# Kernel tuning notes

Measured on AMD Instinct MI355X. Metric: run time of the kernel, lower is better.

Reference implementation:

```python
import jax, jax.numpy as jnp
import numpy as np

N = 50000      # nodes
E = 800000     # directed edges (before self-loops)
DX, DF = 128, 128   # x / feat dims, nfeat = DX + DF = 256
NHID = 256
NRES = 100     # policy head outputs NRES + 1


def setup_inputs() -> dict:
    key = jax.random.key(0)
    ks = jax.random.split(key, 12)
    def lin(k, fin, fout):
        s = 1.0 / np.sqrt(fin)
        kw, kb = jax.random.split(k)
        return (jax.random.uniform(kw, (fin, fout), jnp.float32, -s, s),
                jax.random.uniform(kb, (fout,), jnp.float32, -s, s))
    W1, b1 = lin(ks[3], DX + DF, NHID)
    W2, b2 = lin(ks[4], NHID, NHID)
    Wp, bp = lin(ks[5], NHID, NRES + 1)
    Wq, bq = lin(ks[6], NHID, 1)
    return {
        "x": jax.random.normal(ks[0], (N, DX), jnp.float32),
        "feat": jax.random.normal(ks[1], (N, DF), jnp.float32),
        "edge_index": jax.random.randint(ks[2], (2, E), 0, N, dtype=jnp.int64),
        "W1": W1, "b1": b1, "W2": W2, "b2": b2,
        "Wp": Wp, "bp": bp, "Wq": Wq, "bq": bq,
    }


def _gcn_conv(h, row, col, W, b):
    # h: [N, Fin]; row/col already include self-loops
    h = h @ W + b                                        # linear first (as in source)
    deg = jax.ops.segment_sum(jnp.ones_like(row, h.dtype), row, num_segments=N)
    dis = deg ** -0.5                                    # deg >= 1 thanks to self-loops
    norm = dis[row] * dis[col]                           # [E+N]
    # gather-scale-scatter: out[col] += norm * h[row]
    return jax.ops.segment_sum(norm[:, None] * h[row], col, num_segments=N)


def reference(x, feat, edge_index, W1, b1, W2, b2, Wp, bp, Wq, bq):
    loops = jnp.arange(N, dtype=edge_index.dtype)
    row = jnp.concatenate([edge_index[0], loops])
    col = jnp.concatenate([edge_index[1], loops])

    h = jnp.concatenate([x, feat], axis=-1)              # [N, nfeat]
    h = jax.nn.relu(_gcn_conv(h, row, col, W1, b1))      # dropout p=0 -> identity
    h = jax.nn.relu(_gcn_conv(h, row, col, W2, b2))
    g = jnp.max(h, axis=0)                               # global max pool over nodes -> [NHID]
    finx = g @ Wp + bp                                   # [NRES+1]
    finy = g @ Wq + bq                                   # [1]
    return finx, jax.nn.softmax(finx, axis=0), finy
```

## Files before the change

### kernel.cpp

```cpp
#include <hip/hip_runtime.h>

#define N_NODES 50000
#define N_EDGES 800000
#define NHID    256
#define NRES_P1 101

#define NBUCK   196
#define EPB     3125
#define BCAP    6144
#define POOL_BLOCKS 2048
#define LDK     40

typedef unsigned short u16;
typedef unsigned char  u8;
typedef unsigned long long ull;
typedef __attribute__((ext_vector_type(8))) short short8;
typedef __attribute__((ext_vector_type(4))) float f32x4;

static __device__ __forceinline__ unsigned f2bf(float f) {
    unsigned u = __float_as_uint(f);
    return (u + 0x7FFF + ((u >> 16) & 1)) >> 16;
}
static __device__ __forceinline__ float bflo(unsigned p) {
    return __uint_as_float(p << 16);
}
static __device__ __forceinline__ u8 f2fp8(float f) {
    return (u8)(__builtin_amdgcn_cvt_pk_fp8_f32(f, f, 0, false) & 0xff);
}


__global__ __launch_bounds__(256) void k_bcount(
    const int* __restrict__ ei, int* __restrict__ pC, int* __restrict__ pR) {
    __shared__ int cC[NBUCK], cR[NBUCK];
    int b = blockIdx.x, t = threadIdx.x;
    if (t < NBUCK) { cC[t] = 0; cR[t] = 0; }
    __syncthreads();
    int base = b * EPB;
    for (int i = t; i < EPB; i += 256) {
        int r = ei[base + i];
        int c = ei[N_EDGES + base + i];
        atomicAdd(&cR[r >> 8], 1);
        atomicAdd(&cC[c >> 8], 1);
    }
    __syncthreads();
    if (t < NBUCK) { pC[b * NBUCK + t] = cC[t]; pR[b * NBUCK + t] = cR[t]; }
}

__global__ __launch_bounds__(256) void k_bscan(
    const int* __restrict__ pC, const int* __restrict__ pR,
    int* __restrict__ offC, int* __restrict__ offR,
    int* __restrict__ estC, int* __restrict__ estR) {
    __shared__ int totC[NBUCK], totR[NBUCK];
    int t = threadIdx.x;
    if (t < NBUCK) {
        int runC = 0, runR = 0;
        for (int b = 0; b < 256; b += 8) {
            int vc[8], vr[8];
#pragma unroll
            for (int j = 0; j < 8; ++j) {
                vc[j] = pC[(b + j) * NBUCK + t];
                vr[j] = pR[(b + j) * NBUCK + t];
            }
#pragma unroll
            for (int j = 0; j < 8; ++j) {
                offC[t * 256 + b + j] = runC; runC += vc[j];
                offR[t * 256 + b + j] = runR; runR += vr[j];
            }
        }
        totC[t] = runC; totR[t] = runR;
    }
    __syncthreads();
    if (t == 0) {
        int rc = 0, rr = 0;
        for (int k = 0; k < NBUCK; ++k) {
            estC[k] = rc; rc += totC[k];
            estR[k] = rr; rr += totR[k];
        }
        estC[NBUCK] = rc; estR[NBUCK] = rr;
    }
}

__global__ __launch_bounds__(256) void k_bscatter(
    const int* __restrict__ ei, const int* __restrict__ offC,
    const int* __restrict__ offR, const int* __restrict__ estC,
    const int* __restrict__ estR, unsigned* __restrict__ sortC,
    u16* __restrict__ sortR) {
    __shared__ int curC[NBUCK], curR[NBUCK];
    int b = blockIdx.x, t = threadIdx.x;
    if (t < NBUCK) {
        curC[t] = estC[t] + offC[t * 256 + b];
        curR[t] = estR[t] + offR[t * 256 + b];
    }
    __syncthreads();
    int base = b * EPB;
    for (int i = t; i < EPB; i += 256) {
        int r = ei[base + i];
        int c = ei[N_EDGES + base + i];
        int pc = atomicAdd(&curC[c >> 8], 1);
        sortC[pc] = ((unsigned)(c & 255) << 16) | (unsigned)r;
        int pr = atomicAdd(&curR[r >> 8], 1);
        sortR[pr] = (u16)(r & 255);
    }
}

__global__ __launch_bounds__(256) void k_bcsr(
    const unsigned* __restrict__ sortC, const int* __restrict__ estC,
    const u16* __restrict__ sortR, const int* __restrict__ estR,
    int* __restrict__ rowptr, int* __restrict__ rowend,
    int* __restrict__ srcl, float* __restrict__ dis) {
    __shared__ int hist[256], cur[256], excl[256], hist2[256];
    __shared__ int wsum[4], woff[4];
    __shared__ unsigned stg[BCAP];
    int k = blockIdx.x, t = threadIdx.x;
    int lane = t & 63, wid = t >> 6;
    int nloc = min(256, N_NODES - k * 256);
    int es = estC[k], ee = estC[k + 1];
    int ecnt = ee - es;
    int fs = es + k * 256;
    hist[t] = 0; cur[t] = 0; hist2[t] = 0;
    __syncthreads();
    for (int i = t; i < ecnt; i += 256)
        atomicAdd(&hist[sortC[es + i] >> 16], 1);
    {
        int rs = estR[k], rcnt = estR[k + 1] - rs;
        for (int i = t; i < rcnt; i += 256)
            atomicAdd(&hist2[(int)sortR[rs + i]], 1);
    }
    __syncthreads();
    if (t < nloc) dis[k * 256 + t] = rsqrtf((float)(hist2[t] + 1));
    int sv = hist[t] + (t < nloc ? 1 : 0);
    int sc = sv;
#pragma unroll
    for (int off = 1; off < 64; off <<= 1) {
        int y = __shfl_up(sc, off, 64);
        if (lane >= off) sc += y;
    }
    if (lane == 63) wsum[wid] = sc;
    __syncthreads();
    if (t == 0) {
        int r = 0;
#pragma unroll
        for (int w = 0; w < 4; ++w) { woff[w] = r; r += wsum[w]; }
    }
    __syncthreads();
    int ex = woff[wid] + sc - sv;
    excl[t] = ex;
    if (t < nloc) {
        rowptr[k * 256 + t] = fs + ex;
        rowend[k * 256 + t] = fs + ex + hist[t] + 1;
    }
    __syncthreads();
    int tot = ecnt + nloc;
    if (tot <= BCAP) {
        for (int i = t; i < ecnt; i += 256) {
            unsigned v = sortC[es + i];
            int j = v >> 16;
            int p = excl[j] + atomicAdd(&cur[j], 1);
            stg[p] = v & 0xffffu;
        }
        if (t < nloc) stg[excl[t] + hist[t]] = (unsigned)(k * 256 + t);
        __syncthreads();
        for (int i = t; i < tot; i += 256) srcl[fs + i] = (int)stg[i];
    } else {
        for (int i = t; i < ecnt; i += 256) {
            unsigned v = sortC[es + i];
            int j = v >> 16;
            int p = excl[j] + atomicAdd(&cur[j], 1);
            srcl[fs + p] = (int)(v & 0xffffu);
        }
        if (t < nloc) srcl[fs + excl[t] + hist[t]] = k * 256 + t;
    }
}

__global__ void k_prep_w2(const float* __restrict__ W1, const float* __restrict__ W2,
                          u16* __restrict__ W1T, u16* __restrict__ W2T) {
    int tid = blockIdx.x * 256 + threadIdx.x;
    const float* W = (tid < 8192) ? W1 : W2;
    u16* WT = (tid < 8192) ? W1T : W2T;
    int id = tid & 8191;
    int n = id >> 5, k8 = (id & 31) << 3;
    u16 tmp[8];
#pragma unroll
    for (int i = 0; i < 8; ++i) tmp[i] = (u16)f2bf(W[(size_t)(k8 + i) * 256 + n]);
    *(uint4*)&WT[(size_t)n * 256 + k8] = *(uint4*)tmp;
}


template <bool SPLIT, bool W16, bool W8>
__global__ __launch_bounds__(256, 2) void k_gemm_mfma(
    const void* __restrict__ A0v, const float* __restrict__ A1,
    const u16* __restrict__ WT, const float* __restrict__ bias,
    const float* __restrict__ dis, u16* __restrict__ out16,
    u8* __restrict__ out8, int M) {
    __shared__ u16 As[128][LDK];
    __shared__ u16 Bs[256][LDK];
    const int t = threadIdx.x;
    const int m0 = blockIdx.x * 128;
    const int lane = t & 63, wave = t >> 6;
    const int wm = wave & 1, wn = wave >> 1;
    const int lr = lane & 15, kg = lane >> 4;

    f32x4 acc[4][8] = {};

    for (int k0 = 0; k0 < 256; k0 += 32) {
#pragma unroll
        for (int i = 0; i < 2; ++i) {
            int idx = i * 256 + t;
            int row = idx >> 2, kc = (idx & 3) << 3;
            int grow = m0 + row;
            uint4 pk = {0u, 0u, 0u, 0u};
            if (grow < M) {
                if (SPLIT) {
                    int k = k0 + kc;
                    const float* src = (k < 128)
                        ? ((const float*)A0v + (size_t)grow * 128 + k)
                        : (A1 + (size_t)grow * 128 + (k - 128));
                    float4 f0 = *(const float4*)src;
                    float4 f1 = *(const float4*)(src + 4);
                    pk.x = f2bf(f0.x) | (f2bf(f0.y) << 16);
                    pk.y = f2bf(f0.z) | (f2bf(f0.w) << 16);
                    pk.z = f2bf(f1.x) | (f2bf(f1.y) << 16);
                    pk.w = f2bf(f1.z) | (f2bf(f1.w) << 16);
                } else {
                    pk = *(const uint4*)((const u16*)A0v +
                                         (size_t)grow * 256 + k0 + kc);
                }
            }
            *(uint4*)&As[row][kc] = pk;
        }
#pragma unroll
        for (int i = 0; i < 4; ++i) {
            int idx = i * 256 + t;
            int n = idx >> 2, kc = (idx & 3) << 3;
            *(uint4*)&Bs[n][kc] = *(const uint4*)&WT[(size_t)n * 256 + k0 + kc];
        }
        __syncthreads();
        short8 af[4], bf[8];
#pragma unroll
        for (int mi = 0; mi < 4; ++mi)
            af[mi] = *(const short8*)&As[wm * 64 + mi * 16 + lr][kg * 8];
#pragma unroll
        for (int ni = 0; ni < 8; ++ni)
            bf[ni] = *(const short8*)&Bs[wn * 128 + ni * 16 + lr][kg * 8];
#pragma unroll
        for (int mi = 0; mi < 4; ++mi)
#pragma unroll
            for (int ni = 0; ni < 8; ++ni)
                acc[mi][ni] = __builtin_amdgcn_mfma_f32_16x16x32_bf16(
                    af[mi], bf[ni], acc[mi][ni], 0, 0, 0);
        __syncthreads();
    }

    const int orow = m0 + wm * 64;
    const int ocol = wn * 128;
#pragma unroll
    for (int mi = 0; mi < 4; ++mi) {
#pragma unroll
        for (int r = 0; r < 4; ++r) {
            int row = orow + mi * 16 + kg * 4 + r;
            if (row >= M) continue;
            float d = dis[row];
#pragma unroll
            for (int ni = 0; ni < 8; ++ni) {
                int col = ocol + ni * 16 + lr;
                float v = d * (acc[mi][ni][r] + bias[col]);
                if (W16) out16[(size_t)row * 256 + col] = (u16)f2bf(v);
                if (W8)  out8[(size_t)row * 256 + col] = f2fp8(v);
            }
        }
    }
}


static __device__ __forceinline__ void addf8(uint2 v, float* a) {
    auto f0 = __builtin_amdgcn_cvt_pk_f32_fp8((int)v.x, false);
    auto f1 = __builtin_amdgcn_cvt_pk_f32_fp8((int)v.x, true);
    auto f2 = __builtin_amdgcn_cvt_pk_f32_fp8((int)v.y, false);
    auto f3 = __builtin_amdgcn_cvt_pk_f32_fp8((int)v.y, true);
    a[0] += f0[0]; a[1] += f0[1]; a[2] += f1[0]; a[3] += f1[1];
    a[4] += f2[0]; a[5] += f2[1]; a[6] += f3[0]; a[7] += f3[1];
}

static __device__ __forceinline__ void gather_batch16_f8(
    const int* __restrict__ p, const u8* __restrict__ base, float* a) {
    int4 q0 = *(const int4*)p;
    int4 q1 = *(const int4*)(p + 4);
    int4 q2 = *(const int4*)(p + 8);
    int4 q3 = *(const int4*)(p + 12);
    uint2 v0  = *(const uint2*)(base + (size_t)q0.x * 256);
    uint2 v1  = *(const uint2*)(base + (size_t)q0.y * 256);
    uint2 v2  = *(const uint2*)(base + (size_t)q0.z * 256);
    uint2 v3  = *(const uint2*)(base + (size_t)q0.w * 256);
    uint2 v4  = *(const uint2*)(base + (size_t)q1.x * 256);
    uint2 v5  = *(const uint2*)(base + (size_t)q1.y * 256);
    uint2 v6  = *(const uint2*)(base + (size_t)q1.z * 256);
    uint2 v7  = *(const uint2*)(base + (size_t)q1.w * 256);
    uint2 v8  = *(const uint2*)(base + (size_t)q2.x * 256);
    uint2 v9  = *(const uint2*)(base + (size_t)q2.y * 256);
    uint2 v10 = *(const uint2*)(base + (size_t)q2.z * 256);
    uint2 v11 = *(const uint2*)(base + (size_t)q2.w * 256);
    uint2 v12 = *(const uint2*)(base + (size_t)q3.x * 256);
    uint2 v13 = *(const uint2*)(base + (size_t)q3.y * 256);
    uint2 v14 = *(const uint2*)(base + (size_t)q3.z * 256);
    uint2 v15 = *(const uint2*)(base + (size_t)q3.w * 256);
    addf8(v0, a);  addf8(v1, a);  addf8(v2, a);  addf8(v3, a);
    addf8(v4, a);  addf8(v5, a);  addf8(v6, a);  addf8(v7, a);
    addf8(v8, a);  addf8(v9, a);  addf8(v10, a); addf8(v11, a);
    addf8(v12, a); addf8(v13, a); addf8(v14, a); addf8(v15, a);
}

__global__ __launch_bounds__(256) void k_agg_f8(
    const int* __restrict__ rowptr, const int* __restrict__ rowend,
    const int* __restrict__ srcl, const u8* __restrict__ hs,
    const float* __restrict__ dis, u16* __restrict__ out) {
    __shared__ int idxb[4][64];
    int wave = threadIdx.x >> 6;
    int lane = threadIdx.x & 63;
    int half = lane >> 5;
    int c8 = lane & 31;
    int dst = blockIdx.x * 4 + wave;
    if (dst >= N_NODES) return;
    int s = rowptr[dst], e = rowend[dst];
    const u8* base = hs + c8 * 8;
    float a[8] = {0.f, 0.f, 0.f, 0.f, 0.f, 0.f, 0.f, 0.f};
    for (int k0 = s; k0 < e; k0 += 64) {
        int kk = k0 + lane;
        idxb[wave][lane] = (kk < e) ? __builtin_nontemporal_load(&srcl[kk])
                                    : N_NODES;
        int nn = min(64, e - k0);
        for (int j = 0; j < nn; j += 32)
            gather_batch16_f8(&idxb[wave][j + half * 16], base, a);
    }
#pragma unroll
    for (int j = 0; j < 8; ++j) a[j] += __shfl_xor(a[j], 32, 64);
    if (half == 0) {
        float d = dis[dst];
        uint4 p;
        p.x = f2bf(fmaxf(a[0] * d, 0.f)) | (f2bf(fmaxf(a[1] * d, 0.f)) << 16);
        p.y = f2bf(fmaxf(a[2] * d, 0.f)) | (f2bf(fmaxf(a[3] * d, 0.f)) << 16);
        p.z = f2bf(fmaxf(a[4] * d, 0.f)) | (f2bf(fmaxf(a[5] * d, 0.f)) << 16);
        p.w = f2bf(fmaxf(a[6] * d, 0.f)) | (f2bf(fmaxf(a[7] * d, 0.f)) << 16);
        *(uint4*)&out[(size_t)dst * 256 + c8 * 8] = p;
    }
}


static __device__ __forceinline__ ull packmd(float v, int dstid) {
    return ((ull)__float_as_uint(v) << 32) | (unsigned)dstid;
}

__global__ __launch_bounds__(256) void k_agg_pool_f8(
    const int* __restrict__ rowptr, const int* __restrict__ rowend,
    const int* __restrict__ srcl, const u8* __restrict__ hs,
    const float* __restrict__ dis, ull* __restrict__ gpool) {
    __shared__ int idxb[4][64];
    __shared__ ull lm[4][256];
    int wave = threadIdx.x >> 6;
    int lane = threadIdx.x & 63;
    int half = lane >> 5;
    int c8 = lane & 31;
    const u8* base = hs + c8 * 8;
    float m[8] = {0.f, 0.f, 0.f, 0.f, 0.f, 0.f, 0.f, 0.f};
    int   ad[8] = {0, 0, 0, 0, 0, 0, 0, 0};
    for (int dst = blockIdx.x * 4 + wave; dst < N_NODES;
         dst += POOL_BLOCKS * 4) {
        int s = rowptr[dst], e = rowend[dst];
        float a[8] = {0.f, 0.f, 0.f, 0.f, 0.f, 0.f, 0.f, 0.f};
        for (int k0 = s; k0 < e; k0 += 64) {
            int kk = k0 + lane;
            idxb[wave][lane] = (kk < e) ? __builtin_nontemporal_load(&srcl[kk])
                                        : N_NODES;
            int nn = min(64, e - k0);
            for (int j = 0; j < nn; j += 32)
                gather_batch16_f8(&idxb[wave][j + half * 16], base, a);
        }
        float d = dis[dst];
#pragma unroll
        for (int j = 0; j < 8; ++j) {
            float v = (a[j] + __shfl_xor(a[j], 32, 64)) * d;
            if (v > m[j]) { m[j] = v; ad[j] = dst; }
        }
    }
    if (half == 0) {
#pragma unroll
        for (int j = 0; j < 8; ++j) lm[wave][c8 * 8 + j] = packmd(m[j], ad[j]);
    }
    __syncthreads();
    int t = threadIdx.x;
    ull v = lm[0][t];
    v = (lm[1][t] > v) ? lm[1][t] : v;
    v = (lm[2][t] > v) ? lm[2][t] : v;
    v = (lm[3][t] > v) ? lm[3][t] : v;
    atomicMax(&gpool[t], v);
}

__global__ __launch_bounds__(256) void k_fix(
    const ull* __restrict__ gpool, const int* __restrict__ rowptr,
    const int* __restrict__ rowend, const int* __restrict__ srcl,
    const u16* __restrict__ h3, const float* __restrict__ dis,
    float* __restrict__ g) {
    int t = threadIdx.x;
    int dst = (int)(unsigned)(gpool[t] & 0xffffffffull);
    int s = rowptr[dst], e = rowend[dst];
    float sum = 0.f;
    for (int k = s; k < e; ++k) {
        int src = srcl[k];
        sum += bflo((unsigned)h3[(size_t)src * 256 + t]);
    }
    g[t] = fmaxf(dis[dst] * sum, 0.f);
}


__global__ __launch_bounds__(128) void k_head(
    const float* __restrict__ g, const float* __restrict__ Wp,
    const float* __restrict__ bp, const float* __restrict__ Wq,
    const float* __restrict__ bq, float* __restrict__ out) {
    __shared__ float sg[NHID];
    __shared__ float red[128];
    int t = threadIdx.x;
    sg[t] = g[t];
    sg[t + 128] = g[t + 128];
    __syncthreads();

    float v = 0.0f;
    if (t < NRES_P1) {
        float acc = bp[t];
        for (int k = 0; k < NHID; ++k) acc = fmaf(sg[k], Wp[k * NRES_P1 + t], acc);
        out[t] = acc;
        v = acc;
    }
    red[t] = (t < NRES_P1) ? v : -1e30f;
    __syncthreads();
#pragma unroll
    for (int off = 64; off > 0; off >>= 1) {
        if (t < off) red[t] = fmaxf(red[t], red[t + off]);
        __syncthreads();
    }
    float mx = red[0];
    __syncthreads();
    float ex = (t < NRES_P1) ? expf(v - mx) : 0.0f;
    red[t] = ex;
    __syncthreads();
#pragma unroll
    for (int off = 64; off > 0; off >>= 1) {
        if (t < off) red[t] += red[t + off];
        __syncthreads();
    }
    float sum = red[0];
    if (t < NRES_P1) out[NRES_P1 + t] = ex / sum;

    if (t < 64) {
        float a = fmaf(sg[t], Wq[t], 0.f);
        a = fmaf(sg[t + 64],  Wq[t + 64],  a);
        a = fmaf(sg[t + 128], Wq[t + 128], a);
        a = fmaf(sg[t + 192], Wq[t + 192], a);
#pragma unroll
        for (int off = 32; off > 0; off >>= 1) a += __shfl_down(a, off, 64);
        if (t == 0) out[2 * NRES_P1] = a + bq[0];
    }
}


static inline size_t align256(size_t x) { return (x + 255) & ~size_t(255); }

extern "C" void kernel_launch(void* const* d_in, const int* in_sizes, int n_in,
                              void* d_out, int out_size, void* d_ws,
                              size_t ws_size, hipStream_t stream) {
    (void)in_sizes; (void)n_in; (void)out_size; (void)ws_size;
    const float* x    = (const float*)d_in[0];
    const float* feat = (const float*)d_in[1];
    const int*   ei   = (const int*)d_in[2];
    const float* W1   = (const float*)d_in[3];
    const float* b1   = (const float*)d_in[4];
    const float* W2   = (const float*)d_in[5];
    const float* b2   = (const float*)d_in[6];
    const float* Wp   = (const float*)d_in[7];
    const float* bp   = (const float*)d_in[8];
    const float* Wq   = (const float*)d_in[9];
    const float* bq   = (const float*)d_in[10];
    float* out = (float*)d_out;

    char* ws = (char*)d_ws;
    size_t off = 0;
    auto alloc = [&](size_t bytes) {
        void* p = ws + off;
        off = align256(off + bytes);
        return p;
    };
    int*   rowptr = (int*)alloc(4ull * N_NODES);
    int*   rowend = (int*)alloc(4ull * N_NODES);
    int*   srcl   = (int*)alloc(4ull * (N_EDGES + N_NODES));
    int*   estC   = (int*)alloc(4ull * (NBUCK + 1));
    int*   estR   = (int*)alloc(4ull * (NBUCK + 1));
    float* dis    = (float*)alloc(4ull * N_NODES);
    float* g      = (float*)alloc(4ull * NHID);
    ull*   gpool  = (ull*)alloc(8ull * NHID);
    u16*   W1T    = (u16*)alloc(2ull * 256 * 256);
    u16*   W2T    = (u16*)alloc(2ull * 256 * 256);
    u8*    buf1f8 = (u8*)alloc(1ull * (N_NODES + 1) * 256);
    u16*   buf2   = (u16*)alloc(2ull * N_NODES * 256);
    u16*   buf3   = (u16*)alloc(2ull * N_NODES * 256);
    u8*    buf3f8 = (u8*)alloc(1ull * (N_NODES + 1) * 256);

    int*      pC    = (int*)buf2;
    int*      pR    = pC  + 256 * NBUCK;
    int*      offC  = pR  + 256 * NBUCK;
    int*      offR  = offC + 256 * NBUCK;
    unsigned* sortC = (unsigned*)buf3;
    u16*      sortR = (u16*)((char*)buf3 + 4ull * N_EDGES);

    hipMemsetAsync(gpool, 0, 8ull * NHID, stream);
    hipMemsetAsync(buf1f8 + (size_t)N_NODES * 256, 0, 256, stream);
    hipMemsetAsync(buf3f8 + (size_t)N_NODES * 256, 0, 256, stream);

    k_prep_w2<<<64, 256, 0, stream>>>(W1, W2, W1T, W2T);
    k_bcount<<<256, 256, 0, stream>>>(ei, pC, pR);
    k_bscan<<<1, 256, 0, stream>>>(pC, pR, offC, offR, estC, estR);
    k_bscatter<<<256, 256, 0, stream>>>(ei, offC, offR, estC, estR,
                                        sortC, sortR);
    k_bcsr<<<NBUCK, 256, 0, stream>>>(sortC, estC, sortR, estR,
                                      rowptr, rowend, srcl, dis);

    const int gblocks = (N_NODES + 127) / 128;
    k_gemm_mfma<true, false, true><<<gblocks, 256, 0, stream>>>(
        x, feat, W1T, b1, dis, nullptr, buf1f8, N_NODES);
    k_agg_f8<<<(N_NODES + 3) / 4, 256, 0, stream>>>(rowptr, rowend, srcl,
                                                    buf1f8, dis, buf2);
    k_gemm_mfma<false, true, true><<<gblocks, 256, 0, stream>>>(
        buf2, nullptr, W2T, b2, dis, buf3, buf3f8, N_NODES);
    k_agg_pool_f8<<<POOL_BLOCKS, 256, 0, stream>>>(rowptr, rowend, srcl,
                                                   buf3f8, dis, gpool);
    k_fix<<<1, 256, 0, stream>>>(gpool, rowptr, rowend, srcl, buf3, dis, g);

    k_head<<<1, 128, 0, stream>>>(g, Wp, bp, Wq, bq, out);
}
```

Measured before the change: 260.7 us.

## Drop bf16 layer-2 output, recompute argmax columns in fix, use LDS-direct loads

The second GEMM no longer writes a bf16 copy of its output, only fp8. The fix kernel now recomputes each argmax column exactly from the layer-1 aggregate (buf2) and W2T: it uses one block per output feature, gathers dis-weighted neighbour rows, then does a dot product and a bias term. The GEMM loads its tiles with global_load_lds into XOR-swizzled, unpadded shared memory for the bf16 input path and the weights. The memsets are folded into the weight-prep kernel. Together these are meant to cut a 25MB store and extra launches, at the cost of a heavier fix kernel and the correctness risk of the swizzle and LDS-direct addressing.

After: 228.0 us. 1.14x faster.

```diff
diff --git a/kernel.cpp b/kernel.cpp
--- a/kernel.cpp
+++ b/kernel.cpp
@@ -9,7 +9,6 @@
 #define EPB     3125
 #define BCAP    6144
 #define POOL_BLOCKS 2048
-#define LDK     40
 
 typedef unsigned short u16;
 typedef unsigned char  u8;
@@ -173,8 +172,18 @@
 }
 
 __global__ void k_prep_w2(const float* __restrict__ W1, const float* __restrict__ W2,
-                          u16* __restrict__ W1T, u16* __restrict__ W2T) {
+                          u16* __restrict__ W1T, u16* __restrict__ W2T,
+                          ull* __restrict__ gpool, u8* __restrict__ z1,
+                          u8* __restrict__ z2) {
     int tid = blockIdx.x * 256 + threadIdx.x;
+    if (blockIdx.x == 0) {
+        int t = threadIdx.x;
+        gpool[t] = 0ull;
+        if (t < 64) {
+            ((unsigned*)z1)[t] = 0u;
+            ((unsigned*)z2)[t] = 0u;
+        }
+    }
     const float* W = (tid < 8192) ? W1 : W2;
     u16* WT = (tid < 8192) ? W1T : W2T;
     int id = tid & 8191;
@@ -186,14 +195,13 @@
 }
 
 
-template <bool SPLIT, bool W16, bool W8>
+template <bool SPLIT>
 __global__ __launch_bounds__(256, 2) void k_gemm_mfma(
     const void* __restrict__ A0v, const float* __restrict__ A1,
     const u16* __restrict__ WT, const float* __restrict__ bias,
-    const float* __restrict__ dis, u16* __restrict__ out16,
-    u8* __restrict__ out8, int M) {
-    __shared__ u16 As[128][LDK];
-    __shared__ u16 Bs[256][LDK];
+    const float* __restrict__ dis, u8* __restrict__ out8, int M) {
+    __shared__ u16 As[128][32];
+    __shared__ u16 Bs[256][32];
     const int t = threadIdx.x;
     const int m0 = blockIdx.x * 128;
     const int lane = t & 63, wave = t >> 6;
@@ -203,15 +211,16 @@
     f32x4 acc[4][8] = {};
 
     for (int k0 = 0; k0 < 256; k0 += 32) {
-#pragma unroll
-        for (int i = 0; i < 2; ++i) {
-            int idx = i * 256 + t;
-            int row = idx >> 2, kc = (idx & 3) << 3;
-            int grow = m0 + row;
-            uint4 pk = {0u, 0u, 0u, 0u};
-            if (grow < M) {
-                if (SPLIT) {
-                    int k = k0 + kc;
+        if (SPLIT) {
+#pragma unroll
+            for (int i = 0; i < 2; ++i) {
+                int idx = i * 256 + t;
+                int row = idx >> 2, c = idx & 3;
+                int cl = c ^ ((row >> 1) & 3);
+                int grow = m0 + row;
+                uint4 pk = {0u, 0u, 0u, 0u};
+                if (grow < M) {
+                    int k = k0 + cl * 8;
                     const float* src = (k < 128)
                         ? ((const float*)A0v + (size_t)grow * 128 + k)
                         : (A1 + (size_t)grow * 128 + (k - 128));
@@ -221,33 +230,54 @@
                     pk.y = f2bf(f0.z) | (f2bf(f0.w) << 16);
                     pk.z = f2bf(f1.x) | (f2bf(f1.y) << 16);
                     pk.w = f2bf(f1.z) | (f2bf(f1.w) << 16);
-                } else {
-                    pk = *(const uint4*)((const u16*)A0v +
-                                         (size_t)grow * 256 + k0 + kc);
                 }
+                *(uint4*)&As[row][c * 8] = pk;
             }
-            *(uint4*)&As[row][kc] = pk;
+        } else {
+#pragma unroll
+            for (int i = 0; i < 2; ++i) {
+                int idx = i * 256 + t;
+                int row = idx >> 2, c = idx & 3;
+                int cl = c ^ ((row >> 1) & 3);
+                const u16* src = (const u16*)A0v + (size_t)(m0 + row) * 256
+                                 + k0 + cl * 8;
+                __builtin_amdgcn_global_load_lds(
+                    (const __attribute__((address_space(1))) void*)src,
+                    (__attribute__((address_space(3))) void*)
+                        ((char*)&As[0][0] + ((i * 256 + wave * 64) << 4)),
+                    16, 0, 0);
+            }
         }
 #pragma unroll
         for (int i = 0; i < 4; ++i) {
             int idx = i * 256 + t;
-            int n = idx >> 2, kc = (idx & 3) << 3;
-            *(uint4*)&Bs[n][kc] = *(const uint4*)&WT[(size_t)n * 256 + k0 + kc];
-        }
-        __syncthreads();
-        short8 af[4], bf[8];
-#pragma unroll
-        for (int mi = 0; mi < 4; ++mi)
-            af[mi] = *(const short8*)&As[wm * 64 + mi * 16 + lr][kg * 8];
-#pragma unroll
-        for (int ni = 0; ni < 8; ++ni)
-            bf[ni] = *(const short8*)&Bs[wn * 128 + ni * 16 + lr][kg * 8];
+            int row = idx >> 2, c = idx & 3;
+            int cl = c ^ ((row >> 1) & 3);
+            const u16* src = WT + (size_t)row * 256 + k0 + cl * 8;
+            __builtin_amdgcn_global_load_lds(
+                (const __attribute__((address_space(1))) void*)src,
+                (__attribute__((address_space(3))) void*)
+                    ((char*)&Bs[0][0] + ((i * 256 + wave * 64) << 4)),
+                16, 0, 0);
+        }
+        __syncthreads();
+        short8 af[4], bfr[8];
+#pragma unroll
+        for (int mi = 0; mi < 4; ++mi) {
+            int row = wm * 64 + mi * 16 + lr;
+            af[mi] = *(const short8*)&As[row][(kg ^ ((row >> 1) & 3)) * 8];
+        }
+#pragma unroll
+        for (int ni = 0; ni < 8; ++ni) {
+            int row = wn * 128 + ni * 16 + lr;
+            bfr[ni] = *(const short8*)&Bs[row][(kg ^ ((row >> 1) & 3)) * 8];
+        }
 #pragma unroll
         for (int mi = 0; mi < 4; ++mi)
 #pragma unroll
             for (int ni = 0; ni < 8; ++ni)
                 acc[mi][ni] = __builtin_amdgcn_mfma_f32_16x16x32_bf16(
-                    af[mi], bf[ni], acc[mi][ni], 0, 0, 0);
+                    af[mi], bfr[ni], acc[mi][ni], 0, 0, 0);
         __syncthreads();
     }
 
@@ -263,9 +293,8 @@
 #pragma unroll
             for (int ni = 0; ni < 8; ++ni) {
                 int col = ocol + ni * 16 + lr;
-                float v = d * (acc[mi][ni][r] + bias[col]);
-                if (W16) out16[(size_t)row * 256 + col] = (u16)f2bf(v);
-                if (W8)  out8[(size_t)row * 256 + col] = f2fp8(v);
+                out8[(size_t)row * 256 + col] =
+                    f2fp8(d * (acc[mi][ni][r] + bias[col]));
             }
         }
     }
@@ -344,7 +373,6 @@
     }
 }
 
-
 static __device__ __forceinline__ ull packmd(float v, int dstid) {
     return ((ull)__float_as_uint(v) << 32) | (unsigned)dstid;
 }
@@ -397,17 +425,57 @@
 __global__ __launch_bounds__(256) void k_fix(
     const ull* __restrict__ gpool, const int* __restrict__ rowptr,
     const int* __restrict__ rowend, const int* __restrict__ srcl,
-    const u16* __restrict__ h3, const float* __restrict__ dis,
+    const u16* __restrict__ h2, const u16* __restrict__ W2T,
+    const float* __restrict__ b2, const float* __restrict__ dis,
     float* __restrict__ g) {
+    __shared__ float red[256];
+    __shared__ int   sidx[128];
+    __shared__ float sdis[128];
+    __shared__ float Dsh;
+    int b = blockIdx.x;
     int t = threadIdx.x;
-    int dst = (int)(unsigned)(gpool[t] & 0xffffffffull);
+    int dst = (int)(unsigned)(gpool[b] & 0xffffffffull);
     int s = rowptr[dst], e = rowend[dst];
-    float sum = 0.f;
-    for (int k = s; k < e; ++k) {
-        int src = srcl[k];
-        sum += bflo((unsigned)h3[(size_t)src * 256 + t]);
-    }
-    g[t] = fmaxf(dis[dst] * sum, 0.f);
+    int n = e - s;
+    float uk = 0.f;
+    if (t == 0) Dsh = 0.f;
+    for (int c0 = 0; c0 < n; c0 += 128) {
+        int nn = min(128, n - c0);
+        __syncthreads();
+        for (int i = t; i < nn; i += 256) {
+            int sr = srcl[s + c0 + i];
+            sidx[i] = sr; sdis[i] = dis[sr];
+        }
+        __syncthreads();
+        int i = 0;
+        for (; i + 4 <= nn; i += 4) {
+            float v0 = bflo((unsigned)h2[(size_t)sidx[i]     * 256 + t]);
+            float v1 = bflo((unsigned)h2[(size_t)sidx[i + 1] * 256 + t]);
+            float v2 = bflo((unsigned)h2[(size_t)sidx[i + 2] * 256 + t]);
+            float v3 = bflo((unsigned)h2[(size_t)sidx[i + 3] * 256 + t]);
+            uk += sdis[i] * v0 + sdis[i + 1] * v1
+                + sdis[i + 2] * v2 + sdis[i + 3] * v3;
+        }
+        for (; i < nn; ++i)
+            uk += sdis[i] * bflo((unsigned)h2[(size_t)sidx[i] * 256 + t]);
+        if (t == 0) {
+            float dl = 0.f;
+            for (int q = 0; q < nn; ++q) dl += sdis[q];
+            Dsh += dl;
+        }
+    }
+    float w = bflo((unsigned)W2T[(size_t)b * 256 + t]);
+    red[t] = uk * w;
+    __syncthreads();
+#pragma unroll
+    for (int off = 128; off > 0; off >>= 1) {
+        if (t < off) red[t] += red[t + off];
+        __syncthreads();
+    }
+    if (t == 0) {
+        float val = red[0] + b2[b] * Dsh;
+        g[b] = fmaxf(dis[dst] * val, 0.f);
+    }
 }
 
 
@@ -499,21 +567,19 @@
     u16*   W2T    = (u16*)alloc(2ull * 256 * 256);
     u8*    buf1f8 = (u8*)alloc(1ull * (N_NODES + 1) * 256);
     u16*   buf2   = (u16*)alloc(2ull * N_NODES * 256);
-    u16*   buf3   = (u16*)alloc(2ull * N_NODES * 256);
     u8*    buf3f8 = (u8*)alloc(1ull * (N_NODES + 1) * 256);
+    alloc(64 * 1024);
 
     int*      pC    = (int*)buf2;
     int*      pR    = pC  + 256 * NBUCK;
     int*      offC  = pR  + 256 * NBUCK;
     int*      offR  = offC + 256 * NBUCK;
-    unsigned* sortC = (unsigned*)buf3;
-    u16*      sortR = (u16*)((char*)buf3 + 4ull * N_EDGES);
-
-    hipMemsetAsync(gpool, 0, 8ull * NHID, stream);
-    hipMemsetAsync(buf1f8 + (size_t)N_NODES * 256, 0, 256, stream);
-    hipMemsetAsync(buf3f8 + (size_t)N_NODES * 256, 0, 256, stream);
-
-    k_prep_w2<<<64, 256, 0, stream>>>(W1, W2, W1T, W2T);
+    unsigned* sortC = (unsigned*)(offR + 256 * NBUCK);
+    u16*      sortR = (u16*)(sortC + N_EDGES);
+
+    k_prep_w2<<<64, 256, 0, stream>>>(W1, W2, W1T, W2T, gpool,
+                                      buf1f8 + (size_t)N_NODES * 256,
+                                      buf3f8 + (size_t)N_NODES * 256);
     k_bcount<<<256, 256, 0, stream>>>(ei, pC, pR);
     k_bscan<<<1, 256, 0, stream>>>(pC, pR, offC, offR, estC, estR);
     k_bscatter<<<256, 256, 0, stream>>>(ei, offC, offR, estC, estR,
@@ -522,15 +588,16 @@
                                       rowptr, rowend, srcl, dis);
 
     const int gblocks = (N_NODES + 127) / 128;
-    k_gemm_mfma<true, false, true><<<gblocks, 256, 0, stream>>>(
-        x, feat, W1T, b1, dis, nullptr, buf1f8, N_NODES);
+    k_gemm_mfma<true><<<gblocks, 256, 0, stream>>>(
+        x, feat, W1T, b1, dis, buf1f8, N_NODES);
     k_agg_f8<<<(N_NODES + 3) / 4, 256, 0, stream>>>(rowptr, rowend, srcl,
                                                     buf1f8, dis, buf2);
-    k_gemm_mfma<false, true, true><<<gblocks, 256, 0, stream>>>(
-        buf2, nullptr, W2T, b2, dis, buf3, buf3f8, N_NODES);
+    k_gemm_mfma<false><<<gblocks, 256, 0, stream>>>(
+        buf2, nullptr, W2T, b2, dis, buf3f8, N_NODES);
     k_agg_pool_f8<<<POOL_BLOCKS, 256, 0, stream>>>(rowptr, rowend, srcl,
                                                    buf3f8, dis, gpool);
-    k_fix<<<1, 256, 0, stream>>>(gpool, rowptr, rowend, srcl, buf3, dis, g);
+    k_fix<<<NHID, 256, 0, stream>>>(gpool, rowptr, rowend, srcl,
+                                    buf2, W2T, b2, dis, g);
 
     k_head<<<1, 128, 0, stream>>>(g, Wp, bp, Wq, bq, out);
 }
```
